# Optimization experiments

Measured on AMD Instinct MI355X. Metric: run time of the kernel, lower is better.

Reference implementation:

```python
import jax, jax.numpy as jnp
import numpy as np

EPS = 1e-5
SLOPE = 0.2


def _conv3d(x, w, stride):
    # x: [B, Cin, D, H, W], w: [Cout, Cin, 3, 3, 3]
    return jax.lax.conv_general_dilated(
        x, w, window_strides=(stride, stride, stride),
        padding=[(1, 1), (1, 1), (1, 1)],
        dimension_numbers=("NCDHW", "OIDHW", "NCDHW"))


def _layernorm_c(y, g, b):
    # LayerNorm over the channel (feature) dim, matching nn.LayerNorm(C) on [N, C]
    mu = jnp.mean(y, axis=1, keepdims=True)
    var = jnp.mean((y - mu) ** 2, axis=1, keepdims=True)
    yn = (y - mu) * jax.lax.rsqrt(var + EPS)
    return yn * g[None, :, None, None, None] + b[None, :, None, None, None]


def _leaky(y):
    return jnp.where(y > 0, y, SLOPE * y)


def _block(x, m, w, g, b, stride):
    # x already zero at inactive sites, so dense conv == sparse gather-scatter conv
    y = _conv3d(x, w, stride)
    if stride > 1:
        # strided SparseConv3d: output active iff any input in 3x3x3 window active
        ones_k = jnp.ones((1, 1, 3, 3, 3), x.dtype)
        m = (_conv3d(m, ones_k, stride) > 0).astype(x.dtype)
    y = _leaky(_layernorm_c(y, g, b))
    return y * m, m


def setup_inputs() -> dict:
    key = jax.random.key(0)
    ks = jax.random.split(key, 16)
    B, D = 2, 64
    x = jax.random.normal(ks[0], (B, 3, D, D, D), jnp.float32)
    mask = jax.random.randint(ks[1], (B, D, D, D), 0, 2) > 0
    chans = [(3, 64), (64, 128), (128, 256), (256, 512)]
    inp = {"x": x, "mask": mask}
    for i, (ci, co) in enumerate(chans):
        inp[f"w{i+1}"] = jax.random.normal(ks[2 + 3 * i], (co, ci, 3, 3, 3), jnp.float32) * 0.05
        inp[f"g{i+1}"] = jnp.ones((co,), jnp.float32)
        inp[f"b{i+1}"] = jnp.zeros((co,), jnp.float32)
    return inp


def reference(x, mask, w1, g1, b1, w2, g2, b2, w3, g3, b3, w4, g4, b4):
    m = mask.astype(x.dtype)[:, None]          # [B,1,D,H,W]
    x = x * m                                  # zero inactive sites
    # SubMConv3d: active set unchanged (stride 1)
    y, m = _block(x, m, w1, g1, b1, 1)
    y, m = _block(y, m, w2, g2, b2, 2)
    y, m = _block(y, m, w3, g3, b3, 2)
    y, m = _block(y, m, w4, g4, b4, 2)
    # .dense() fills inactive sites with 0 (already the case), then amax over D,H,W
    return jnp.max(y, axis=(2, 3, 4))          # [B, 512]
```

## Files before the change

### kernel.cpp

```cpp
#include <hip/hip_runtime.h>
#include <hip/hip_bf16.h>
#include <stdint.h>

#define EPS 1e-5f
#define SLOPE 0.2f

typedef __attribute__((ext_vector_type(8))) short short8;
typedef __attribute__((ext_vector_type(4))) float f32x4;

static __device__ inline ushort f2bf(float f) {
  __hip_bfloat16 h = __float2bfloat16(f);
  return *reinterpret_cast<ushort*>(&h);
}

static __device__ inline short8 u4_to_s8(uint a, uint b, uint c, uint d) {
  union { uint4 u; short8 s; } cv;
  cv.u.x = a; cv.u.y = b; cv.u.z = c; cv.u.w = d;
  return cv.s;
}

__global__ void mask_detect_k(const uint8_t* __restrict__ raw, int nbytes,
                              unsigned* __restrict__ flag) {
  unsigned local = 0;
  for (int i = blockIdx.x * blockDim.x + threadIdx.x; i < nbytes;
       i += gridDim.x * blockDim.x)
    if (i & 3) local |= raw[i];
  if (local) atomicOr(flag, 1u);
}

__global__ void xclm_k(const float* __restrict__ x, const uint8_t* __restrict__ raw,
                       const unsigned* __restrict__ flag,
                       uint8_t* __restrict__ m1, ushort* __restrict__ xclp) {
  int id = blockIdx.x * blockDim.x + threadIdx.x;
  if (id >= 2 * 262144) return;
  uint8_t v;
  if (*flag) {
    v = raw[id];
  } else {
    size_t j = 4 * (size_t)id;
    v = (uint8_t)(raw[j] | raw[j + 1] | raw[j + 2] | raw[j + 3]);
  }
  v = v ? 1 : 0;
  m1[id] = v;
  float mk = (float)v;
  int b  = id >> 18;
  int sp = id & 262143;
  int xx = sp & 63, yy = (sp >> 6) & 63, zz = sp >> 12;
  size_t base = (size_t)b * 3 * 262144 + sp;
  float x0 = x[base] * mk;
  float x1 = x[base + 262144] * mk;
  float x2 = x[base + 2 * 262144] * mk;
  uint2 u;
  u.x = ((uint)f2bf(x1) << 16) | (uint)f2bf(x0);
  u.y = (uint)f2bf(x2);
  size_t pidx = ((((size_t)(b * 66 + zz + 1)) * 66 + (yy + 1)) * 66 + (xx + 1)) * 4;
  *reinterpret_cast<uint2*>(xclp + pidx) = u;
}

__global__ void mask_down_k(const uint8_t* __restrict__ mi,
                            uint8_t* __restrict__ mo, int DIN) {
  int W = DIN >> 1;
  int id = blockIdx.x * blockDim.x + threadIdx.x;
  int total = 2 * W * W * W;
  if (id >= total) return;
  int xo = id % W; int t = id / W;
  int yo = t % W;  t /= W;
  int zo = t % W;  int b = t / W;
  int any = 0;
  for (int dz = 0; dz < 3; ++dz) {
    int z = 2 * zo + dz - 1; if (z < 0 || z >= DIN) continue;
    for (int dy = 0; dy < 3; ++dy) {
      int y = 2 * yo + dy - 1; if (y < 0 || y >= DIN) continue;
      for (int dx = 0; dx < 3; ++dx) {
        int x = 2 * xo + dx - 1; if (x < 0 || x >= DIN) continue;
        any |= mi[(((size_t)b * DIN + z) * DIN + y) * DIN + x];
      }
    }
  }
  mo[id] = any ? 1 : 0;
}

__global__ void wprep_k(const float* __restrict__ w1, const float* __restrict__ w2,
                        const float* __restrict__ w3, const float* __restrict__ w4,
                        ushort* __restrict__ wb1, ushort* __restrict__ wb2,
                        ushort* __restrict__ wb3, ushort* __restrict__ wb4) {
  int id = blockIdx.x * blockDim.x + threadIdx.x;
  if (id < 8192) {
    int k = id & 127, c = id >> 7;
    int tap = k >> 2, ci = k & 3;
    float v = (tap < 27 && ci < 3) ? w1[c * 81 + ci * 27 + tap] : 0.f;
    wb1[id] = f2bf(v);
    return;
  }
  id -= 8192;
  if (id < 128 * 1728) {
    int kn = id % 1728, c = id / 1728;
    int off = kn >> 6, ci = kn & 63;
    wb2[(size_t)c * 1728 + kn] = f2bf(w2[(size_t)c * 1728 + ci * 27 + off]);
    return;
  }
  id -= 128 * 1728;
  if (id < 256 * 3456) {
    int kn = id % 3456, c = id / 3456;
    int off = kn >> 7, ci = kn & 127;
    wb3[(size_t)c * 3456 + kn] = f2bf(w3[(size_t)c * 3456 + ci * 27 + off]);
    return;
  }
  id -= 256 * 3456;
  if (id < 512 * 6912) {
    int kn = id % 6912, c = id / 6912;
    int off = kn >> 8, ci = kn & 255;
    wb4[(size_t)c * 6912 + kn] = f2bf(w4[(size_t)c * 6912 + ci * 27 + off]);
  }
}

__global__ __launch_bounds__(256) void conv1_gemm(
    const ushort* __restrict__ xclp,
    const ushort* __restrict__ wb1,
    const float* __restrict__ gamma,
    const float* __restrict__ beta,
    const uint8_t* __restrict__ msk,
    ushort* __restrict__ out)
{
  const int t    = threadIdx.x;
  const int lane = t & 63;
  const int wave = t >> 6;
  const int c8   = lane >> 4;

  const int bid = blockIdx.x;
  const int yp = bid & 31;
  const int zq = (bid >> 5) & 15;
  const int b  = bid >> 9;
  const int y0 = yp * 2;
  const int z0 = zq * 4;

  __shared__ uint2 tile[1584];

  const uint2* xin = reinterpret_cast<const uint2*>(xclp);
  const long gbase = (((long)(b * 66 + z0)) * 66 + y0) * 66;
  for (int e = t; e < 1584; e += 256) {
    int p = e / 264;
    tile[e] = xin[gbase + e + p * 4092];
  }

  int eoff[2][2][2];
#pragma unroll
  for (int kb = 0; kb < 2; ++kb)
#pragma unroll
    for (int kh = 0; kh < 2; ++kh)
#pragma unroll
      for (int p = 0; p < 2; ++p) {
        int tap = kb * 16 + kh * 8 + c8 * 2 + p;
        int off = 0;
        if (tap < 27) {
          int dz = tap / 9, rr = tap - dz * 9;
          int dy = rr / 3, dx = rr - dy * 3;
          off = dz * 264 + dy * 66 + dx;
        }
        eoff[kb][kh][p] = off;
      }

  int ebase[2];
#pragma unroll
  for (int nf = 0; nf < 2; ++nf) {
    int nl = wave * 32 + nf * 16 + (lane & 15);
    ebase[nf] = (nl >> 6) * 66 + (nl & 63);
  }

  float gr[4][4], br_[4][4];
#pragma unroll
  for (int mf = 0; mf < 4; ++mf) {
    int cb = mf * 16 + c8 * 4;
    f32x4 gv  = *reinterpret_cast<const f32x4*>(gamma + cb);
    f32x4 bv2 = *reinterpret_cast<const f32x4*>(beta + cb);
#pragma unroll
    for (int r = 0; r < 4; ++r) { gr[mf][r] = gv[r]; br_[mf][r] = bv2[r]; }
  }

  __syncthreads();

  for (int zi = 0; zi < 4; ++zi) {
    const int zsh = zi * 264;
    f32x4 acc[4][2];
#pragma unroll
    for (int i = 0; i < 4; ++i)
#pragma unroll
      for (int j = 0; j < 2; ++j) acc[i][j] = (f32x4)(0.f);

#pragma unroll
    for (int kb = 0; kb < 2; ++kb) {
      short8 afr[4][2];
#pragma unroll
      for (int mf = 0; mf < 4; ++mf)
#pragma unroll
        for (int kh = 0; kh < 2; ++kh) {
          int row = mf * 16 + (lane & 15);
          int k   = kb * 64 + (c8 + kh * 4) * 8;
          afr[mf][kh] = *reinterpret_cast<const short8*>(wb1 + row * 128 + k);
        }
#pragma unroll
      for (int nf = 0; nf < 2; ++nf)
#pragma unroll
        for (int kh = 0; kh < 2; ++kh) {
          uint2 v0 = tile[ebase[nf] + zsh + eoff[kb][kh][0]];
          uint2 v1 = tile[ebase[nf] + zsh + eoff[kb][kh][1]];
          short8 bfr = u4_to_s8(v0.x, v0.y, v1.x, v1.y);
#pragma unroll
          for (int mf = 0; mf < 4; ++mf)
            acc[mf][nf] = __builtin_amdgcn_mfma_f32_16x16x32_bf16(
                afr[mf][kh], bfr, acc[mf][nf], 0, 0, 0);
        }
    }

    const int z = z0 + zi;
    const int voxbase = ((b * 64 + z) * 64 + y0) * 64;
#pragma unroll
    for (int nf = 0; nf < 2; ++nf) {
      float s = 0.f, sq = 0.f;
#pragma unroll
      for (int mf = 0; mf < 4; ++mf)
#pragma unroll
        for (int r = 0; r < 4; ++r) {
          float v = acc[mf][nf][r];
          s += v; sq += v * v;
        }
      s  += __shfl_xor(s, 16);  sq += __shfl_xor(sq, 16);
      s  += __shfl_xor(s, 32);  sq += __shfl_xor(sq, 32);
      const float mean = s * (1.f / 64.f);
      const float var  = sq * (1.f / 64.f) - mean * mean;
      const float rstd = rsqrtf(var + EPS);
      const int vox = voxbase + wave * 32 + nf * 16 + (lane & 15);
      const float mk = msk[vox] ? 1.f : 0.f;
#pragma unroll
      for (int mf = 0; mf < 4; ++mf) {
        uint2 u;
        float r0 = (acc[mf][nf][0] - mean) * rstd * gr[mf][0] + br_[mf][0];
        float r1 = (acc[mf][nf][1] - mean) * rstd * gr[mf][1] + br_[mf][1];
        float r2 = (acc[mf][nf][2] - mean) * rstd * gr[mf][2] + br_[mf][2];
        float r3 = (acc[mf][nf][3] - mean) * rstd * gr[mf][3] + br_[mf][3];
        r0 = (r0 > 0.f ? r0 : SLOPE * r0) * mk;
        r1 = (r1 > 0.f ? r1 : SLOPE * r1) * mk;
        r2 = (r2 > 0.f ? r2 : SLOPE * r2) * mk;
        r3 = (r3 > 0.f ? r3 : SLOPE * r3) * mk;
        u.x = ((uint)f2bf(r1) << 16) | (uint)f2bf(r0);
        u.y = ((uint)f2bf(r3) << 16) | (uint)f2bf(r2);
        *reinterpret_cast<uint2*>(out + (size_t)vox * 64 + mf * 16 + c8 * 4) = u;
      }
    }
  }
}

__global__ __launch_bounds__(256) void conv2_gemm(
    const ushort* __restrict__ in,
    const ushort* __restrict__ wbf,
    const float* __restrict__ gamma,
    const float* __restrict__ beta,
    const uint8_t* __restrict__ msk,
    ushort* __restrict__ out,
    const ushort* __restrict__ zpage)
{
  constexpr int CIN = 64, DIN = 64, S = 2;
  constexpr int W = 32, K = 1728, NT = 27, LW = 5;

  const int t    = threadIdx.x;
  const int lane = t & 63;
  const int wave = t >> 6;
  int bid = blockIdx.x;
  bid = (bid & 7) * 64 + (bid >> 3);
  const int n0 = bid * 128;

  __shared__ short As[2][128 * 64];
  __shared__ short Bs[2][128 * 64];
  __shared__ float lnS[4][4][16];
  __shared__ float lnQ[4][4][16];

  int zb[4], yb[4], xb[4], kc8[4], swz[4];
  size_t bb[4];
  const ushort* aptr[4];
#pragma unroll
  for (int j = 0; j < 4; ++j) {
    int q  = t + 256 * j;
    int nl = q >> 3, kc = q & 7;
    kc8[j] = kc * 8;
    swz[j] = nl * 64 + ((kc ^ (nl & 7)) << 3);
    int ngv = n0 + nl;
    int xo = ngv & (W - 1), yo = (ngv >> LW) & (W - 1),
        zo = (ngv >> (2 * LW)) & (W - 1), b = ngv >> (3 * LW);
    xb[j] = xo * S; yb[j] = yo * S; zb[j] = zo * S;
    bb[j] = (size_t)b * CIN * DIN * DIN * DIN;
    aptr[j] = wbf + (size_t)nl * K + kc * 8;
  }

  short8 ar[4], br[4];

  auto LOADK = [&](int kb) {
    const int off = kb;
    const int dz = off / 9, rr = off % 9;
    const int dy = rr / 3, dx = rr % 3;
#pragma unroll
    for (int j = 0; j < 4; ++j) {
      ar[j] = *reinterpret_cast<const short8*>(aptr[j] + kb * 64);
      int zin = zb[j] + dz - 1;
      int yin = yb[j] + dy - 1;
      int xin = xb[j] + dx - 1;
      bool ok = ((unsigned)zin < (unsigned)DIN) &&
                ((unsigned)yin < (unsigned)DIN) &&
                ((unsigned)xin < (unsigned)DIN);
      const ushort* p = ok
          ? in + bb[j] + (((size_t)zin * DIN + yin) * DIN + xin) * CIN + kc8[j]
          : zpage;
      br[j] = *reinterpret_cast<const short8*>(p);
    }
  };

  auto WRITEK = [&](int buf) {
#pragma unroll
    for (int j = 0; j < 4; ++j) {
      *reinterpret_cast<short8*>(&As[buf][swz[j]]) = ar[j];
      *reinterpret_cast<short8*>(&Bs[buf][swz[j]]) = br[j];
    }
  };

  f32x4 acc[4][4];
#pragma unroll
  for (int i = 0; i < 4; ++i)
#pragma unroll
    for (int j = 0; j < 4; ++j) acc[i][j] = (f32x4)(0.f);

  const int wm = (wave & 1) * 64;
  const int wn = (wave >> 1) * 64;

  LOADK(0);
  for (int kb = 0; kb < NT; ++kb) {
    const int buf = kb & 1;
    WRITEK(buf);
    if (kb + 1 < NT) LOADK(kb + 1);
    __syncthreads();

    short8 afr[4][2], bfr[4][2];
#pragma unroll
    for (int mf = 0; mf < 4; ++mf)
#pragma unroll
      for (int kh = 0; kh < 2; ++kh) {
        int row  = wm + mf * 16 + (lane & 15);
        int slot = (lane >> 4) + kh * 4;
        afr[mf][kh] = *reinterpret_cast<const short8*>(
            &As[buf][row * 64 + ((slot ^ (row & 7)) << 3)]);
      }
#pragma unroll
    for (int nf = 0; nf < 4; ++nf)
#pragma unroll
      for (int kh = 0; kh < 2; ++kh) {
        int row  = wn + nf * 16 + (lane & 15);
        int slot = (lane >> 4) + kh * 4;
        bfr[nf][kh] = *reinterpret_cast<const short8*>(
            &Bs[buf][row * 64 + ((slot ^ (row & 7)) << 3)]);
      }
#pragma unroll
    for (int mf = 0; mf < 4; ++mf)
#pragma unroll
      for (int nf = 0; nf < 4; ++nf)
#pragma unroll
        for (int kh = 0; kh < 2; ++kh)
          acc[mf][nf] = __builtin_amdgcn_mfma_f32_16x16x32_bf16(
              afr[mf][kh], bfr[nf][kh], acc[mf][nf], 0, 0, 0);
  }

  float sv[4], qv[4];
#pragma unroll
  for (int nf = 0; nf < 4; ++nf) {
    float s = 0.f, sq = 0.f;
#pragma unroll
    for (int mf = 0; mf < 4; ++mf)
#pragma unroll
      for (int r = 0; r < 4; ++r) {
        float v = acc[mf][nf][r];
        s += v; sq += v * v;
      }
    s  += __shfl_xor(s, 16);  sq += __shfl_xor(sq, 16);
    s  += __shfl_xor(s, 32);  sq += __shfl_xor(sq, 32);
    sv[nf] = s; qv[nf] = sq;
  }
  if (lane < 16) {
#pragma unroll
    for (int nf = 0; nf < 4; ++nf) {
      lnS[wave][nf][lane] = sv[nf];
      lnQ[wave][nf][lane] = qv[nf];
    }
  }
  __syncthreads();

  float gr[4][4], br_[4][4];
#pragma unroll
  for (int mf = 0; mf < 4; ++mf) {
    int cb = wm + mf * 16 + ((lane >> 4) << 2);
    f32x4 gv = *reinterpret_cast<const f32x4*>(gamma + cb);
    f32x4 bv = *reinterpret_cast<const f32x4*>(beta + cb);
#pragma unroll
    for (int r = 0; r < 4; ++r) { gr[mf][r] = gv[r]; br_[mf][r] = bv[r]; }
  }

#pragma unroll
  for (int nf = 0; nf < 4; ++nf) {
    const float s  = sv[nf] + lnS[wave ^ 1][nf][lane & 15];
    const float sq = qv[nf] + lnQ[wave ^ 1][nf][lane & 15];
    const float mean = s * (1.f / 128.f);
    const float var  = sq * (1.f / 128.f) - mean * mean;
    const float rstd = rsqrtf(var + EPS);
    const int vox = n0 + wn + nf * 16 + (lane & 15);
    const float mk = msk[vox] ? 1.f : 0.f;
#pragma unroll
    for (int mf = 0; mf < 4; ++mf) {
      uint2 u;
      float r0 = (acc[mf][nf][0] - mean) * rstd * gr[mf][0] + br_[mf][0];
      float r1 = (acc[mf][nf][1] - mean) * rstd * gr[mf][1] + br_[mf][1];
      float r2 = (acc[mf][nf][2] - mean) * rstd * gr[mf][2] + br_[mf][2];
      float r3 = (acc[mf][nf][3] - mean) * rstd * gr[mf][3] + br_[mf][3];
      r0 = (r0 > 0.f ? r0 : SLOPE * r0) * mk;
      r1 = (r1 > 0.f ? r1 : SLOPE * r1) * mk;
      r2 = (r2 > 0.f ? r2 : SLOPE * r2) * mk;
      r3 = (r3 > 0.f ? r3 : SLOPE * r3) * mk;
      u.x = ((uint)f2bf(r1) << 16) | (uint)f2bf(r0);
      u.y = ((uint)f2bf(r3) << 16) | (uint)f2bf(r2);
      *reinterpret_cast<uint2*>(out + (size_t)vox * 128 + wm + mf * 16 +
                                ((lane >> 4) << 2)) = u;
    }
  }
}

template <int CIN, int COUT, int DIN, int S, int L2CIN, int SPLITK>
__global__ __launch_bounds__(256) void conv_gemm(
    const ushort* __restrict__ in,
    const ushort* __restrict__ wbf,
    float* __restrict__ rawout,
    const ushort* __restrict__ zpage)
{
  constexpr int W  = DIN / S;
  constexpr int K  = 27 * CIN;
  constexpr int NT = K / 64;
  constexpr int NTS = NT / SPLITK;
  constexpr int LW = (W == 32) ? 5 : (W == 16) ? 4 : 3;
  constexpr size_t NVOX = (size_t)2 * W * W * W;

  const int t    = threadIdx.x;
  const int lane = t & 63;
  const int wave = t >> 6;
  const int n0   = blockIdx.x * 128;
  const int m0   = blockIdx.y * 128;
  const int kb0  = blockIdx.z * NTS;
  float* rawp = rawout + (size_t)blockIdx.z * NVOX * COUT;

  __shared__ short As[2][128 * 64];
  __shared__ short Bs[2][128 * 64];

  int zb[4], yb[4], xb[4], kc8[4], swz[4];
  size_t bb[4];
  const ushort* aptr[4];
#pragma unroll
  for (int j = 0; j < 4; ++j) {
    int q  = t + 256 * j;
    int nl = q >> 3, kc = q & 7;
    kc8[j] = kc * 8;
    swz[j] = nl * 64 + ((kc ^ (nl & 7)) << 3);
    int ng = n0 + nl;
    int xo = ng & (W - 1), yo = (ng >> LW) & (W - 1),
        zo = (ng >> (2 * LW)) & (W - 1), b = ng >> (3 * LW);
    xb[j] = xo * S; yb[j] = yo * S; zb[j] = zo * S;
    bb[j] = (size_t)b * CIN * DIN * DIN * DIN;
    aptr[j] = wbf + (size_t)(m0 + nl) * K + kc * 8;
  }

  short8 ar[4], br[4];

  auto LOADK = [&](int kb) {
    const int off = (kb * 64) >> L2CIN;
    const int ci0 = (kb * 64) & (CIN - 1);
    const int dz = off / 9, rr = off % 9;
    const int dy = rr / 3, dx = rr % 3;
#pragma unroll
    for (int j = 0; j < 4; ++j) {
      ar[j] = *reinterpret_cast<const short8*>(aptr[j] + kb * 64);
      int zin = zb[j] + dz - 1;
      int yin = yb[j] + dy - 1;
      int xin = xb[j] + dx - 1;
      bool ok = ((unsigned)zin < (unsigned)DIN) &&
                ((unsigned)yin < (unsigned)DIN) &&
                ((unsigned)xin < (unsigned)DIN);
      const ushort* p = ok
          ? in + bb[j] + (((size_t)zin * DIN + yin) * DIN + xin) * CIN + ci0 + kc8[j]
          : zpage;
      br[j] = *reinterpret_cast<const short8*>(p);
    }
  };

  auto WRITEK = [&](int buf) {
#pragma unroll
    for (int j = 0; j < 4; ++j) {
      *reinterpret_cast<short8*>(&As[buf][swz[j]]) = ar[j];
      *reinterpret_cast<short8*>(&Bs[buf][swz[j]]) = br[j];
    }
  };

  f32x4 acc[4][4];
#pragma unroll
  for (int i = 0; i < 4; ++i)
#pragma unroll
    for (int j = 0; j < 4; ++j) acc[i][j] = (f32x4)(0.f);

  const int wm = (wave & 1) * 64;
  const int wn = (wave >> 1) * 64;

  LOADK(kb0);
  for (int kb = kb0; kb < kb0 + NTS; ++kb) {
    const int buf = (kb - kb0) & 1;
    WRITEK(buf);
    if (kb + 1 < kb0 + NTS) LOADK(kb + 1);
    __syncthreads();

    short8 afr[4][2], bfr[4][2];
#pragma unroll
    for (int mf = 0; mf < 4; ++mf)
#pragma unroll
      for (int kh = 0; kh < 2; ++kh) {
        int row  = wm + mf * 16 + (lane & 15);
        int slot = (lane >> 4) + kh * 4;
        afr[mf][kh] = *reinterpret_cast<const short8*>(
            &As[buf][row * 64 + ((slot ^ (row & 7)) << 3)]);
      }
#pragma unroll
    for (int nf = 0; nf < 4; ++nf)
#pragma unroll
      for (int kh = 0; kh < 2; ++kh) {
        int row  = wn + nf * 16 + (lane & 15);
        int slot = (lane >> 4) + kh * 4;
        bfr[nf][kh] = *reinterpret_cast<const short8*>(
            &Bs[buf][row * 64 + ((slot ^ (row & 7)) << 3)]);
      }
#pragma unroll
    for (int mf = 0; mf < 4; ++mf)
#pragma unroll
      for (int nf = 0; nf < 4; ++nf)
#pragma unroll
        for (int kh = 0; kh < 2; ++kh)
          acc[mf][nf] = __builtin_amdgcn_mfma_f32_16x16x32_bf16(
              afr[mf][kh], bfr[nf][kh], acc[mf][nf], 0, 0, 0);
  }

#pragma unroll
  for (int mf = 0; mf < 4; ++mf)
#pragma unroll
    for (int nf = 0; nf < 4; ++nf) {
      int mg = m0 + wm + mf * 16 + ((lane >> 4) << 2);
      int ng = n0 + wn + nf * 16 + (lane & 15);
      *reinterpret_cast<f32x4*>(&rawp[(size_t)ng * COUT + mg]) = acc[mf][nf];
    }
}

template <int C, int NPART, bool BF16OUT>
__global__ __launch_bounds__(256) void ln_mask_k(
    const float* __restrict__ raw,
    const float* __restrict__ gamma,
    const float* __restrict__ beta,
    const uint8_t* __restrict__ msk,
    void* __restrict__ outv, int nvox)
{
  constexpr int E = C / 64;
  const int lane = threadIdx.x & 63;
  const int vox  = blockIdx.x * 4 + (threadIdx.x >> 6);
  if (vox >= nvox) return;

  const size_t stride = (size_t)nvox * C;
  const float* p = raw + (size_t)vox * C;
  float v[E];
  float s = 0.f, sq = 0.f;
#pragma unroll
  for (int e = 0; e < E; ++e) {
    float acc = 0.f;
#pragma unroll
    for (int pt = 0; pt < NPART; ++pt) acc += p[pt * stride + e * 64 + lane];
    v[e] = acc;
    s += acc; sq += acc * acc;
  }
#pragma unroll
  for (int off = 32; off; off >>= 1) {
    s  += __shfl_xor(s, off);
    sq += __shfl_xor(sq, off);
  }
  const float mean = s / (float)C;
  const float var  = sq / (float)C - mean * mean;
  const float rstd = rsqrtf(var + EPS);
  const float mk   = msk[vox] ? 1.f : 0.f;

#pragma unroll
  for (int e = 0; e < E; ++e) {
    int c = e * 64 + lane;
    float r = (v[e] - mean) * rstd * gamma[c] + beta[c];
    r = (r > 0.f ? r : SLOPE * r) * mk;
    if (BF16OUT)
      ((ushort*)outv)[(size_t)vox * C + c] = f2bf(r);
    else
      ((float*)outv)[(size_t)vox * C + c] = r;
  }
}

template <int NPART>
__global__ __launch_bounds__(256) void ln4max_k(
    const float* __restrict__ raw,
    const float* __restrict__ gamma,
    const float* __restrict__ beta,
    const uint8_t* __restrict__ msk,
    float* __restrict__ pm)
{
  const int t    = threadIdx.x;
  const int lane = t & 63;
  const int wave = t >> 6;
  const int grp  = blockIdx.x;
  const size_t stride = (size_t)1024 * 512;

  float gg[8], bb_[8];
#pragma unroll
  for (int e = 0; e < 8; ++e) {
    int c = e * 64 + lane;
    gg[e] = gamma[c]; bb_[e] = beta[c];
  }

  float vmax[8];
#pragma unroll
  for (int e = 0; e < 8; ++e) vmax[e] = -1e30f;

  for (int it = 0; it < 16; ++it) {
    const int vox = grp * 64 + wave * 16 + it;
    const float* p = raw + (size_t)vox * 512;
    float v[8];
    float s = 0.f, sq = 0.f;
#pragma unroll
    for (int e = 0; e < 8; ++e) {
      float a = 0.f;
#pragma unroll
      for (int pt = 0; pt < NPART; ++pt) a += p[pt * stride + e * 64 + lane];
      v[e] = a; s += a; sq += a * a;
    }
#pragma unroll
    for (int off = 32; off; off >>= 1) {
      s  += __shfl_xor(s, off);
      sq += __shfl_xor(sq, off);
    }
    const float mean = s * (1.f / 512.f);
    const float var  = sq * (1.f / 512.f) - mean * mean;
    const float rstd = rsqrtf(var + EPS);
    const float mk   = msk[vox] ? 1.f : 0.f;
#pragma unroll
    for (int e = 0; e < 8; ++e) {
      float r = (v[e] - mean) * rstd * gg[e] + bb_[e];
      r = (r > 0.f ? r : SLOPE * r) * mk;
      vmax[e] = fmaxf(vmax[e], r);
    }
  }

  __shared__ float red[4][512];
#pragma unroll
  for (int e = 0; e < 8; ++e) red[wave][e * 64 + lane] = vmax[e];
  __syncthreads();
  for (int c = t; c < 512; c += 256) {
    float m = fmaxf(fmaxf(red[0][c], red[1][c]), fmaxf(red[2][c], red[3][c]));
    pm[(size_t)grp * 512 + c] = m;
  }
}

__global__ void rmax2_k(const float* __restrict__ pm, float* __restrict__ out) {
  const int b = blockIdx.x;
  const int c = threadIdx.x;
  float m = -1e30f;
  for (int g = 0; g < 8; ++g) m = fmaxf(m, pm[((size_t)b * 8 + g) * 512 + c]);
  out[b * 512 + c] = m;
}

extern "C" void kernel_launch(void* const* d_in, const int* in_sizes, int n_in,
                              void* d_out, int out_size, void* d_ws, size_t ws_size,
                              hipStream_t stream) {
  const float*   x    = (const float*)d_in[0];
  const uint8_t* mraw = (const uint8_t*)d_in[1];
  const float* w1 = (const float*)d_in[2];
  const float* g1 = (const float*)d_in[3];
  const float* b1 = (const float*)d_in[4];
  const float* w2 = (const float*)d_in[5];
  const float* g2 = (const float*)d_in[6];
  const float* b2 = (const float*)d_in[7];
  const float* w3 = (const float*)d_in[8];
  const float* g3 = (const float*)d_in[9];
  const float* b3 = (const float*)d_in[10];
  const float* w4 = (const float*)d_in[11];
  const float* g4 = (const float*)d_in[12];
  const float* b4 = (const float*)d_in[13];
  float* out = (float*)d_out;
  char*  ws  = (char*)d_ws;

  const size_t ZP   = 0;
  const size_t T1   = 256;
  const size_t R3b  = 67109120;
  const size_t T2   = 92274944;
  const size_t T3   = 109052160;
  const size_t PM   = 113246464;
  const size_t XCLP = 113279232;
  const size_t XCLP_BYTES = 4600064;
  const size_t WB1  = XCLP + XCLP_BYTES;
  const size_t WB2  = WB1 + 16384;
  const size_t WB3  = WB2 + 442368;
  const size_t WB4  = WB3 + 1769472;
  const size_t M1   = WB4 + 7077888;
  const size_t M2   = M1 + 524288;
  const size_t M3   = M2 + 65536;
  const size_t M4   = M3 + 8192;

  unsigned* flag = (unsigned*)(ws + ZP);
  const ushort* zpage = (const ushort*)(ws + ZP + 16);
  ushort* t1   = (ushort*)(ws + T1);
  float*  r3   = (float*)(ws + R3b);
  float*  r4   = (float*)(ws + R3b + 16777216);
  ushort* t2   = (ushort*)(ws + T2);
  ushort* t3   = (ushort*)(ws + T3);
  float*  pm   = (float*)(ws + PM);
  ushort* xclp = (ushort*)(ws + XCLP);
  ushort* wb1  = (ushort*)(ws + WB1);
  ushort* wb2  = (ushort*)(ws + WB2);
  ushort* wb3  = (ushort*)(ws + WB3);
  ushort* wb4  = (ushort*)(ws + WB4);
  uint8_t* m1  = (uint8_t*)(ws + M1);
  uint8_t* m2  = (uint8_t*)(ws + M2);
  uint8_t* m3  = (uint8_t*)(ws + M3);
  uint8_t* m4  = (uint8_t*)(ws + M4);

  const int NM1 = 2 * 64 * 64 * 64;

  hipMemsetAsync(ws + ZP, 0, 64, stream);
  hipMemsetAsync(ws + XCLP, 0, XCLP_BYTES, stream);
  mask_detect_k<<<256, 256, 0, stream>>>(mraw, NM1, flag);
  xclm_k<<<NM1 / 256, 256, 0, stream>>>(x, mraw, flag, m1, xclp);
  mask_down_k<<<(2 * 32 * 32 * 32 + 255) / 256, 256, 0, stream>>>(m1, m2, 64);
  mask_down_k<<<(2 * 16 * 16 * 16 + 255) / 256, 256, 0, stream>>>(m2, m3, 32);
  mask_down_k<<<(2 * 8 * 8 * 8 + 255) / 256, 256, 0, stream>>>(m3, m4, 16);

  wprep_k<<<18176, 256, 0, stream>>>(w1, w2, w3, w4, wb1, wb2, wb3, wb4);

  conv1_gemm<<<1024, 256, 0, stream>>>(xclp, wb1, g1, b1, m1, t1);

  conv2_gemm<<<512, 256, 0, stream>>>(t1, wb2, g2, b2, m2, t2, zpage);

  conv_gemm<128, 256, 32, 2, 7, 2><<<dim3(64, 2, 2), 256, 0, stream>>>(t2, wb3, r3, zpage);
  ln_mask_k<256, 2, true><<<8192 / 4, 256, 0, stream>>>(r3, g3, b3, m3, t3, 8192);

  conv_gemm<256, 512, 16, 2, 8, 4><<<dim3(8, 4, 4), 256, 0, stream>>>(t3, wb4, r4, zpage);
  ln4max_k<4><<<16, 256, 0, stream>>>(r4, g4, b4, m4, pm);

  rmax2_k<<<2, 512, 0, stream>>>(pm, out);

  (void)in_sizes; (void)n_in; (void)out_size; (void)ws_size;
}
```

Baseline: 199.6 us.

## Load weight fragments directly from global memory and halve voxel tile for conv3/conv4

The conv2 and generic conv GEMM kernels no longer stage the weight (A) operand through shared memory. Each lane now reads its MFMA A fragments straight from global memory, which removes the A stores to LDS and half the LDS footprint. The generic conv_gemm also gains a BN template parameter, and conv3/conv4 launch with a 64-voxel N tile, doubling the grid to improve occupancy and CU coverage. The cost is uncoalesced or cached global reads of weights inside the inner loop, with no prefetch overlap for A, plus less reuse per block.

Measured after the change: 279.7 us. 40.1% more time.

```diff
diff --git a/kernel.cpp b/kernel.cpp
--- a/kernel.cpp
+++ b/kernel.cpp
@@ -265,18 +265,17 @@
   const int t    = threadIdx.x;
   const int lane = t & 63;
   const int wave = t >> 6;
+  const int c8   = lane >> 4;
   int bid = blockIdx.x;
   bid = (bid & 7) * 64 + (bid >> 3);
   const int n0 = bid * 128;
 
-  __shared__ short As[2][128 * 64];
   __shared__ short Bs[2][128 * 64];
   __shared__ float lnS[4][4][16];
   __shared__ float lnQ[4][4][16];
 
   int zb[4], yb[4], xb[4], kc8[4], swz[4];
   size_t bb[4];
-  const ushort* aptr[4];
 #pragma unroll
   for (int j = 0; j < 4; ++j) {
     int q  = t + 256 * j;
@@ -288,10 +287,17 @@
         zo = (ngv >> (2 * LW)) & (W - 1), b = ngv >> (3 * LW);
     xb[j] = xo * S; yb[j] = yo * S; zb[j] = zo * S;
     bb[j] = (size_t)b * CIN * DIN * DIN * DIN;
-    aptr[j] = wbf + (size_t)nl * K + kc * 8;
-  }
-
-  short8 ar[4], br[4];
+  }
+
+  const int wm = (wave & 1) * 64;
+  const int wn = (wave >> 1) * 64;
+
+  const ushort* pa[4];
+#pragma unroll
+  for (int mf = 0; mf < 4; ++mf)
+    pa[mf] = wbf + (size_t)(wm + mf * 16 + (lane & 15)) * K + c8 * 8;
+
+  short8 br[4];
 
   auto LOADK = [&](int kb) {
     const int off = kb;
@@ -299,7 +305,6 @@
     const int dy = rr / 3, dx = rr % 3;
 #pragma unroll
     for (int j = 0; j < 4; ++j) {
-      ar[j] = *reinterpret_cast<const short8*>(aptr[j] + kb * 64);
       int zin = zb[j] + dz - 1;
       int yin = yb[j] + dy - 1;
       int xin = xb[j] + dx - 1;
@@ -315,10 +320,8 @@
 
   auto WRITEK = [&](int buf) {
 #pragma unroll
-    for (int j = 0; j < 4; ++j) {
-      *reinterpret_cast<short8*>(&As[buf][swz[j]]) = ar[j];
+    for (int j = 0; j < 4; ++j)
       *reinterpret_cast<short8*>(&Bs[buf][swz[j]]) = br[j];
-    }
   };
 
   f32x4 acc[4][4];
@@ -326,9 +329,6 @@
   for (int i = 0; i < 4; ++i)
 #pragma unroll
     for (int j = 0; j < 4; ++j) acc[i][j] = (f32x4)(0.f);
-
-  const int wm = (wave & 1) * 64;
-  const int wn = (wave >> 1) * 64;
 
   LOADK(0);
   for (int kb = 0; kb < NT; ++kb) {
@@ -341,12 +341,8 @@
 #pragma unroll
     for (int mf = 0; mf < 4; ++mf)
 #pragma unroll
-      for (int kh = 0; kh < 2; ++kh) {
-        int row  = wm + mf * 16 + (lane & 15);
-        int slot = (lane >> 4) + kh * 4;
-        afr[mf][kh] = *reinterpret_cast<const short8*>(
-            &As[buf][row * 64 + ((slot ^ (row & 7)) << 3)]);
-      }
+      for (int kh = 0; kh < 2; ++kh)
+        afr[mf][kh] = *reinterpret_cast<const short8*>(pa[mf] + kb * 64 + kh * 32);
 #pragma unroll
     for (int nf = 0; nf < 4; ++nf)
 #pragma unroll
@@ -428,7 +424,7 @@
   }
 }
 
-template <int CIN, int COUT, int DIN, int S, int L2CIN, int SPLITK>
+template <int CIN, int COUT, int DIN, int S, int L2CIN, int SPLITK, int BN>
 __global__ __launch_bounds__(256) void conv_gemm(
     const ushort* __restrict__ in,
     const ushort* __restrict__ wbf,
@@ -441,23 +437,23 @@
   constexpr int NTS = NT / SPLITK;
   constexpr int LW = (W == 32) ? 5 : (W == 16) ? 4 : 3;
   constexpr size_t NVOX = (size_t)2 * W * W * W;
+  constexpr int NFC = BN / 32;
 
   const int t    = threadIdx.x;
   const int lane = t & 63;
   const int wave = t >> 6;
-  const int n0   = blockIdx.x * 128;
+  const int c8   = lane >> 4;
+  const int n0   = blockIdx.x * BN;
   const int m0   = blockIdx.y * 128;
   const int kb0  = blockIdx.z * NTS;
   float* rawp = rawout + (size_t)blockIdx.z * NVOX * COUT;
 
-  __shared__ short As[2][128 * 64];
-  __shared__ short Bs[2][128 * 64];
-
-  int zb[4], yb[4], xb[4], kc8[4], swz[4];
-  size_t bb[4];
-  const ushort* aptr[4];
-#pragma unroll
-  for (int j = 0; j < 4; ++j) {
+  __shared__ short Bs[2][BN * 64];
+
+  int zb[NFC], yb[NFC], xb[NFC], kc8[NFC], swz[NFC];
+  size_t bb[NFC];
+#pragma unroll
+  for (int j = 0; j < NFC; ++j) {
     int q  = t + 256 * j;
     int nl = q >> 3, kc = q & 7;
     kc8[j] = kc * 8;
@@ -467,10 +463,17 @@
         zo = (ng >> (2 * LW)) & (W - 1), b = ng >> (3 * LW);
     xb[j] = xo * S; yb[j] = yo * S; zb[j] = zo * S;
     bb[j] = (size_t)b * CIN * DIN * DIN * DIN;
-    aptr[j] = wbf + (size_t)(m0 + nl) * K + kc * 8;
-  }
-
-  short8 ar[4], br[4];
+  }
+
+  const int wm = (wave & 1) * 64;
+  const int wn = (wave >> 1) * (BN / 2);
+
+  const ushort* pa[4];
+#pragma unroll
+  for (int mf = 0; mf < 4; ++mf)
+    pa[mf] = wbf + (size_t)(m0 + wm + mf * 16 + (lane & 15)) * K + c8 * 8;
+
+  short8 br[NFC];
 
   auto LOADK = [&](int kb) {
     const int off = (kb * 64) >> L2CIN;
@@ -478,8 +481,7 @@
     const int dz = off / 9, rr = off % 9;
     const int dy = rr / 3, dx = rr % 3;
 #pragma unroll
-    for (int j = 0; j < 4; ++j) {
-      ar[j] = *reinterpret_cast<const short8*>(aptr[j] + kb * 64);
+    for (int j = 0; j < NFC; ++j) {
       int zin = zb[j] + dz - 1;
       int yin = yb[j] + dy - 1;
       int xin = xb[j] + dx - 1;
@@ -495,20 +497,15 @@
 
   auto WRITEK = [&](int buf) {
 #pragma unroll
-    for (int j = 0; j < 4; ++j) {
-      *reinterpret_cast<short8*>(&As[buf][swz[j]]) = ar[j];
+    for (int j = 0; j < NFC; ++j)
       *reinterpret_cast<short8*>(&Bs[buf][swz[j]]) = br[j];
-    }
   };
 
-  f32x4 acc[4][4];
+  f32x4 acc[4][NFC];
 #pragma unroll
   for (int i = 0; i < 4; ++i)
 #pragma unroll
-    for (int j = 0; j < 4; ++j) acc[i][j] = (f32x4)(0.f);
-
-  const int wm = (wave & 1) * 64;
-  const int wn = (wave >> 1) * 64;
+    for (int j = 0; j < NFC; ++j) acc[i][j] = (f32x4)(0.f);
 
   LOADK(kb0);
   for (int kb = kb0; kb < kb0 + NTS; ++kb) {
@@ -517,18 +514,14 @@
     if (kb + 1 < kb0 + NTS) LOADK(kb + 1);
     __syncthreads();
 
-    short8 afr[4][2], bfr[4][2];
+    short8 afr[4][2], bfr[NFC][2];
 #pragma unroll
     for (int mf = 0; mf < 4; ++mf)
 #pragma unroll
-      for (int kh = 0; kh < 2; ++kh) {
-        int row  = wm + mf * 16 + (lane & 15);
-        int slot = (lane >> 4) + kh * 4;
-        afr[mf][kh] = *reinterpret_cast<const short8*>(
-            &As[buf][row * 64 + ((slot ^ (row & 7)) << 3)]);
-      }
-#pragma unroll
-    for (int nf = 0; nf < 4; ++nf)
+      for (int kh = 0; kh < 2; ++kh)
+        afr[mf][kh] = *reinterpret_cast<const short8*>(pa[mf] + kb * 64 + kh * 32);
+#pragma unroll
+    for (int nf = 0; nf < NFC; ++nf)
 #pragma unroll
       for (int kh = 0; kh < 2; ++kh) {
         int row  = wn + nf * 16 + (lane & 15);
@@ -539,7 +532,7 @@
 #pragma unroll
     for (int mf = 0; mf < 4; ++mf)
 #pragma unroll
-      for (int nf = 0; nf < 4; ++nf)
+      for (int nf = 0; nf < NFC; ++nf)
 #pragma unroll
         for (int kh = 0; kh < 2; ++kh)
           acc[mf][nf] = __builtin_amdgcn_mfma_f32_16x16x32_bf16(
@@ -549,7 +542,7 @@
 #pragma unroll
   for (int mf = 0; mf < 4; ++mf)
 #pragma unroll
-    for (int nf = 0; nf < 4; ++nf) {
+    for (int nf = 0; nf < NFC; ++nf) {
       int mg = m0 + wm + mf * 16 + ((lane >> 4) << 2);
       int ng = n0 + wn + nf * 16 + (lane & 15);
       *reinterpret_cast<f32x4*>(&rawp[(size_t)ng * COUT + mg]) = acc[mf][nf];
@@ -746,10 +739,12 @@
 
   conv2_gemm<<<512, 256, 0, stream>>>(t1, wb2, g2, b2, m2, t2, zpage);
 
-  conv_gemm<128, 256, 32, 2, 7, 2><<<dim3(64, 2, 2), 256, 0, stream>>>(t2, wb3, r3, zpage);
+  conv_gemm<128, 256, 32, 2, 7, 2, 64><<<dim3(128, 2, 2), 256, 0, stream>>>(
+      t2, wb3, r3, zpage);
   ln_mask_k<256, 2, true><<<8192 / 4, 256, 0, stream>>>(r3, g3, b3, m3, t3, 8192);
 
-  conv_gemm<256, 512, 16, 2, 8, 4><<<dim3(8, 4, 4), 256, 0, stream>>>(t3, wb4, r4, zpage);
+  conv_gemm<256, 512, 16, 2, 8, 4, 64><<<dim3(16, 4, 4), 256, 0, stream>>>(
+      t3, wb4, r4, zpage);
   ln4max_k<4><<<16, 256, 0, stream>>>(r4, g4, b4, m4, pm);
 
   rmax2_k<<<2, 512, 0, stream>>>(pm, out);
```
